# Optimization experiments

Hardware: AMD Instinct MI355X
Metric: run time of the kernel (lower is better)

## Reference

```python
import jax, jax.numpy as jnp
import numpy as np

N, D_IN, D_HID, D_OUT = 16384, 512, 2048, 512
NUM_BANDS, RANK, ALPHA = 4, 16, 32
SCALING = ALPHA / RANK  # 2.0


def setup_inputs() -> dict:
    key = jax.random.key(0)
    ks = jax.random.split(key, 10)
    x = jax.random.normal(ks[0], (N, D_IN), dtype=jnp.float32)
    bw = jax.random.uniform(ks[1], (N, NUM_BANDS), dtype=jnp.float32)
    band_weights = bw / jnp.sum(bw, axis=-1, keepdims=True)  # rows sum to 1
    s_in = 1.0 / np.sqrt(D_IN)
    s_hid = 1.0 / np.sqrt(D_HID)
    return {
        "x": x,
        "band_weights": band_weights,
        "W1": jax.random.normal(ks[2], (D_IN, D_HID), dtype=jnp.float32) * s_in,
        "b1": jax.random.normal(ks[3], (D_HID,), dtype=jnp.float32) * 0.01,
        "W2": jax.random.normal(ks[4], (D_HID, D_OUT), dtype=jnp.float32) * s_hid,
        "b2": jax.random.normal(ks[5], (D_OUT,), dtype=jnp.float32) * 0.01,
        "lora_fc1_A": jax.random.normal(ks[6], (NUM_BANDS, D_IN, RANK), dtype=jnp.float32) * s_in,
        "lora_fc1_B": jax.random.normal(ks[7], (NUM_BANDS, RANK, D_HID), dtype=jnp.float32) * 0.02,
        "lora_fc2_A": jax.random.normal(ks[8], (NUM_BANDS, D_HID, RANK), dtype=jnp.float32) * s_hid,
        "lora_fc2_B": jax.random.normal(ks[9], (NUM_BANDS, RANK, D_OUT), dtype=jnp.float32) * 0.02,
    }


def reference(x, band_weights, W1, b1, W2, b2, lora_fc1_A, lora_fc1_B, lora_fc2_A, lora_fc2_B):
    # shared fc1: [N, hidden]
    h_shared = x @ W1 + b1
    # per-band LoRA down-projection: [N, bands, rank]
    t1 = jnp.einsum('ni,bir->nbr', x, lora_fc1_A)
    # up-project and band-weighted sum fused: [N, hidden]
    delta1 = jnp.einsum('nb,nbr,brh->nh', band_weights, t1, lora_fc1_B) * SCALING
    h = jax.nn.gelu(h_shared + delta1, approximate=False)  # torch GELU is erf-based
    out_shared = h @ W2 + b2
    t2 = jnp.einsum('nh,bhr->nbr', h, lora_fc2_A)
    delta2 = jnp.einsum('nb,nbr,bro->no', band_weights, t2, lora_fc2_B) * SCALING
    return out_shared + delta2
```

## Files before the change

### kernel.cpp

```cpp
#include <hip/hip_runtime.h>
#include <hip/hip_bf16.h>

#define DEV __device__ __forceinline__
#define AS1 __attribute__((address_space(1)))
#define AS3 __attribute__((address_space(3)))

typedef __attribute__((ext_vector_type(8))) short bf16x8;
typedef __attribute__((ext_vector_type(4))) float f32x4;

static constexpr int NR   = 16384;
static constexpr int DIN  = 512;
static constexpr int DHID = 2048;
static constexpr int DOUT = 512;
static constexpr int LR   = 64;
static constexpr int K1   = DIN + LR;
static constexpr int K2   = DHID + LR;

DEV unsigned short f2bf(float f) {
  unsigned u = __float_as_uint(f);
  u += 0x7fffu + ((u >> 16) & 1u);
  return (unsigned short)(u >> 16);
}

DEV float fast_gelu(float v) {
  float x2 = v * v;
  float a  = -v * __builtin_fmaf(0.10294324f, x2, 2.30220817f);
  float t  = exp2f(a);
  return v * __builtin_amdgcn_rcpf(1.0f + t);
}

template<int N> DEV void wvm() {
  asm volatile("s_waitcnt vmcnt(%0)" :: "i"(N) : "memory");
}

DEV void tconv_dev(const float* in, unsigned short* out, int C, int LDO, int CO,
                   int bx, int by, float (*t)[33], int tid) {
  int bc = bx * 32, br = by * 32;
  int tx = tid & 31, ty = tid >> 5;
  #pragma unroll
  for (int i = 0; i < 32; i += 8)
    t[ty + i][tx] = in[(size_t)(br + ty + i) * C + bc + tx];
  __syncthreads();
  #pragma unroll
  for (int i = 0; i < 32; i += 8)
    out[(size_t)(bc + ty + i) * LDO + CO + br + tx] = f2bf(t[tx][ty + i]);
}

__global__ __launch_bounds__(256) void prep_kernel(
    const float* __restrict__ W1, const float* __restrict__ B1,
    const float* __restrict__ W2, const float* __restrict__ B2,
    unsigned short* __restrict__ W1cT, unsigned short* __restrict__ W2cT,
    const float* __restrict__ A1, const float* __restrict__ A2,
    unsigned short* __restrict__ A1T, unsigned short* __restrict__ A2T) {
  __shared__ float t[32][33];
  const int b = blockIdx.x, tid = threadIdx.x;
  if (b < 1024) {
    tconv_dev(W1, W1cT, 2048, K1, 0, b & 63, b >> 6, t, tid);
  } else if (b < 2048) {
    int bi = b - 1024;
    tconv_dev(W2, W2cT, 512, K2, 0, bi & 15, bi >> 4, t, tid);
  } else if (b < 2176) {
    int bi = b - 2048;
    tconv_dev(B1, W1cT, 2048, K1, 512, bi & 63, bi >> 6, t, tid);
  } else if (b < 2208) {
    int bi = b - 2176;
    tconv_dev(B2, W2cT, 512, K2, 2048, bi & 15, bi >> 4, t, tid);
  } else if (b < 2336) {
    int i2 = (b - 2208) * 256 + tid;
    int j = i2 / DIN, i = i2 - j * DIN;
    A1T[i2] = f2bf(A1[((size_t)(j >> 4) * DIN + i) * 16 + (j & 15)]);
  } else {
    int i2 = (b - 2336) * 256 + tid;
    int j = i2 / DHID, i = i2 - j * DHID;
    A2T[i2] = f2bf(A2[((size_t)(j >> 4) * DHID + i) * 16 + (j & 15)]);
  }
}

__global__ __launch_bounds__(256) void u1cvt_kernel(
    const float* __restrict__ x, const float* __restrict__ bw,
    const unsigned short* __restrict__ A1T, unsigned short* __restrict__ xaug) {
  __shared__ __align__(16) unsigned short lX[64 * 64];
  __shared__ __align__(16) unsigned short lW[64 * 64];
  const int tid = threadIdx.x;
  const int w = tid >> 6, lane = tid & 63;
  const int bm = blockIdx.x * 64;
  const int l15 = lane & 15;
  const int kc0 = ((lane >> 4) ^ (lane & 7)) * 8;
  const int kc1 = (((lane >> 4) + 4) ^ (lane & 7)) * 8;

  f32x4 acc[4] = {};

  for (int kt = 0; kt < 8; ++kt) {
    #pragma unroll
    for (int i = 0; i < 2; ++i) {
      int row = i * 32 + w * 8 + (lane >> 3);
      __builtin_amdgcn_global_load_lds(
          (const AS1 void*)(A1T + (size_t)row * DIN + kt * 64
                              + (((lane & 7) ^ (row & 7)) * 8)),
          (AS3 void*)(lW + (i * 32 + w * 8) * 64 + lane * 8), 16, 0, 0);
    }
    #pragma unroll
    for (int p = 0; p < 4; ++p) {
      int row = p * 16 + (tid >> 4);
      int col = (tid & 15) * 4;
      float4 v = *(const float4*)(x + (size_t)(bm + row) * DIN + kt * 64 + col);
      uint2 o;
      o.x = (unsigned)f2bf(v.x) | ((unsigned)f2bf(v.y) << 16);
      o.y = (unsigned)f2bf(v.z) | ((unsigned)f2bf(v.w) << 16);
      *(uint2*)(xaug + (size_t)(bm + row) * K1 + kt * 64 + col) = o;
      char* p3 = (char*)lX + row * 128 + (((col >> 3) ^ (row & 7)) << 4) + ((col & 7) << 1);
      *(uint2*)p3 = o;
    }
    __syncthreads();
    bf16x8 af0 = *(const bf16x8*)(lX + (w * 16 + l15) * 64 + kc0);
    bf16x8 af1 = *(const bf16x8*)(lX + (w * 16 + l15) * 64 + kc1);
    #pragma unroll
    for (int n = 0; n < 4; ++n) {
      bf16x8 b0 = *(const bf16x8*)(lW + (n * 16 + l15) * 64 + kc0);
      bf16x8 b1 = *(const bf16x8*)(lW + (n * 16 + l15) * 64 + kc1);
      acc[n] = __builtin_amdgcn_mfma_f32_16x16x32_bf16(af0, b0, acc[n], 0, 0, 0);
      acc[n] = __builtin_amdgcn_mfma_f32_16x16x32_bf16(af1, b1, acc[n], 0, 0, 0);
    }
    __syncthreads();
  }

  #pragma unroll
  for (int n = 0; n < 4; ++n) {
    int col = n * 16 + l15;
    #pragma unroll
    for (int r = 0; r < 4; ++r) {
      int row = bm + w * 16 + ((lane >> 4) << 2) + r;
      float v = acc[n][r] * 2.0f * bw[row * 4 + n];
      xaug[(size_t)row * K1 + 512 + col] = f2bf(v);
    }
  }
}

template<int BM, int BN, int WAVES, int K, int EPI, int NBY>
__global__ __launch_bounds__(WAVES * 64, 2) void gemmx_kernel(
    const unsigned short* __restrict__ A, int lda,
    const unsigned short* __restrict__ B, int ldb,
    const float* __restrict__ bias,
    void* __restrict__ outp, int ldo, int ocol) {
  constexpr int THREADS = WAVES * 64;
  constexpr int NT = K / 64;
  constexpr int AL = BM * 4 / THREADS;
  constexpr int BL = BN * 4 / THREADS;
  constexpr int HA = (BM / 2) * 64;
  constexpr int HB = (BN / 2) * 64;
  constexpr int MQ = BM / 64;
  constexpr int WC = WAVES / 2;
  static_assert(NT >= 2 && AL >= 1 && BL >= 1 && (BN / 2) / WC == 32, "geometry");
  __shared__ __align__(16) unsigned short lA[4 * HA];
  __shared__ __align__(16) unsigned short lB[4 * HB];

  const int tid  = threadIdx.x;
  const int w    = tid >> 6, lane = tid & 63;
  const int wr   = w / WC, wc = w % WC;
  const int bid  = blockIdx.x;
  const int tt   = bid >> 3;
  const int by   = tt % NBY;
  const int bx   = (tt / NBY) * 8 + (bid & 7);
  const int bm   = bx * BM, bn = by * BN;
  const int l15  = lane & 15;
  const int kc0  = ((lane >> 4) ^ (lane & 7)) * 8;
  const int kc1  = (((lane >> 4) + 4) ^ (lane & 7)) * 8;

  f32x4 acc[2][2][MQ][2] = {};
  bf16x8 af[2][MQ][2];
  bf16x8 bfv[2][2];

  auto stageA = [&](int buf, int half, int t) {
    #pragma unroll
    for (int i = 0; i < AL; ++i) {
      int row = w * (AL * 8) + i * 8 + (lane >> 3);
      __builtin_amdgcn_global_load_lds(
          (const AS1 void*)(A + (size_t)(bm + half * (BM / 2) + row) * lda
                              + (size_t)t * 64 + (((lane & 7) ^ (row & 7)) * 8)),
          (AS3 void*)(lA + (buf * 2 + half) * HA + (w * AL + i) * 512),
          16, 0, 0);
    }
  };
  auto stageB = [&](int buf, int half, int t) {
    #pragma unroll
    for (int i = 0; i < BL; ++i) {
      int row = w * (BL * 8) + i * 8 + (lane >> 3);
      __builtin_amdgcn_global_load_lds(
          (const AS1 void*)(B + (size_t)(bn + half * (BN / 2) + row) * ldb
                              + (size_t)t * 64 + (((lane & 7) ^ (row & 7)) * 8)),
          (AS3 void*)(lB + (buf * 2 + half) * HB + (w * BL + i) * 512),
          16, 0, 0);
    }
  };
  auto ldAall = [&](int buf) {
    #pragma unroll
    for (int mh = 0; mh < 2; ++mh) {
      const unsigned short* sA = lA + (buf * 2 + mh) * HA;
      #pragma unroll
      for (int m = 0; m < MQ; ++m) {
        int ro = (wr * (BM / 4) + m * 16 + l15) * 64;
        af[mh][m][0] = *(const bf16x8*)(sA + ro + kc0);
        af[mh][m][1] = *(const bf16x8*)(sA + ro + kc1);
      }
    }
  };
  auto ldB = [&](int buf, int nh) {
    const unsigned short* sB = lB + (buf * 2 + nh) * HB;
    #pragma unroll
    for (int n = 0; n < 2; ++n) {
      int ro = (wc * 32 + n * 16 + l15) * 64;
      bfv[n][0] = *(const bf16x8*)(sB + ro + kc0);
      bfv[n][1] = *(const bf16x8*)(sB + ro + kc1);
    }
  };

#define MFMA_Q(mh, nh)                                                           \
  _Pragma("unroll")                                                              \
  for (int m = 0; m < MQ; ++m)                                                   \
    _Pragma("unroll")                                                            \
    for (int n = 0; n < 2; ++n) {                                                \
      acc[mh][nh][m][n] = __builtin_amdgcn_mfma_f32_16x16x32_bf16(               \
          af[mh][m][0], bfv[n][0], acc[mh][nh][m][n], 0, 0, 0);                  \
      acc[mh][nh][m][n] = __builtin_amdgcn_mfma_f32_16x16x32_bf16(               \
          af[mh][m][1], bfv[n][1], acc[mh][nh][m][n], 0, 0, 0);                  \
    }

#define BAR() __builtin_amdgcn_s_barrier()

  stageA(0, 0, 0); stageA(0, 1, 0); stageB(0, 0, 0); stageB(0, 1, 0);
  wvm<BL>();
  BAR();

  for (int t = 0; t < NT; ++t) {
    const int buf = t & 1, nb = buf ^ 1;
    const bool more = (t + 1 < NT);
    ldAall(buf);
    ldB(buf, 0);
    if (more) { stageA(nb, 0, t + 1); stageA(nb, 1, t + 1); stageB(nb, 0, t + 1); }
    MFMA_Q(0, 0);
    MFMA_Q(1, 0);
    if (more) wvm<2 * AL + BL>(); else wvm<0>();
    BAR();
    if (more) stageB(nb, 1, t + 1);
    ldB(buf, 1);
    MFMA_Q(0, 1);
    MFMA_Q(1, 1);
    if (more) {
      wvm<BL>();
      BAR();
    }
  }
#undef MFMA_Q
#undef BAR

  float biasv[2][2];
  #pragma unroll
  for (int nh = 0; nh < 2; ++nh)
    #pragma unroll
    for (int n = 0; n < 2; ++n)
      biasv[nh][n] = bias[bn + nh * (BN / 2) + wc * 32 + n * 16 + l15];

  #pragma unroll
  for (int mh = 0; mh < 2; ++mh)
    #pragma unroll
    for (int nh = 0; nh < 2; ++nh)
      #pragma unroll
      for (int m = 0; m < MQ; ++m)
        #pragma unroll
        for (int n = 0; n < 2; ++n) {
          int col  = bn + nh * (BN / 2) + wc * 32 + n * 16 + l15;
          int rowb = bm + mh * (BM / 2) + wr * (BM / 4) + m * 16 + ((lane >> 4) << 2);
          #pragma unroll
          for (int r = 0; r < 4; ++r) {
            float v = acc[mh][nh][m][n][r];
            int row = rowb + r;
            if (EPI == 0) {
              v = fast_gelu(v + biasv[nh][n]);
              ((unsigned short*)outp)[(size_t)row * ldo + ocol + col] = f2bf(v);
            } else {
              v += biasv[nh][n];
              ((float*)outp)[(size_t)row * ldo + col] = v;
            }
          }
        }
}

template<int BM, int BN, int WM, int WN, int K>
__global__ __launch_bounds__(256) void gemmu_kernel(
    const unsigned short* __restrict__ A, int lda,
    const unsigned short* __restrict__ B, int ldb,
    const float* __restrict__ bw,
    unsigned short* __restrict__ outp, int ldo, int ocol) {
  constexpr int WRM = WM / 16, WRN = WN / 16;
  constexpr int NWN = BN / WN;
  constexpr int NT  = K / 64;
  constexpr int NBUF = 3;
  constexpr int AISS = BM * 64 * 2 / 4096;
  constexpr int BISS = BN * 64 * 2 / 4096;
  constexpr int LOADS = AISS + BISS;
  static_assert((BM / WM) * (BN / WN) == 4 && NT >= NBUF, "geometry");
  __shared__ __align__(16) unsigned short lA[NBUF * BM * 64];
  __shared__ __align__(16) unsigned short lB[NBUF * BN * 64];

  const int tid  = threadIdx.x;
  const int wid  = tid >> 6, lane = tid & 63;
  const int wr   = wid / NWN, wc = wid % NWN;
  const int bm   = blockIdx.x * BM, bn = blockIdx.y * BN;
  const int l15  = lane & 15;
  const int kc0  = ((lane >> 4) ^ (lane & 7)) * 8;
  const int kc1  = (((lane >> 4) + 4) ^ (lane & 7)) * 8;

  f32x4 acc[WRM][WRN] = {};

  auto stage = [&](int buf, int t) {
    #pragma unroll
    for (int i = 0; i < AISS; i++) {
      int row = (wid * AISS + i) * 8 + (lane >> 3);
      __builtin_amdgcn_global_load_lds(
          (const AS1 void*)(A + (size_t)(bm + row) * lda + (size_t)t * 64
                              + (((lane & 7) ^ (row & 7)) * 8)),
          (AS3 void*)(lA + buf * (BM * 64) + (wid * AISS + i) * 512), 16, 0, 0);
    }
    #pragma unroll
    for (int i = 0; i < BISS; i++) {
      int row = (wid * BISS + i) * 8 + (lane >> 3);
      __builtin_amdgcn_global_load_lds(
          (const AS1 void*)(B + (size_t)(bn + row) * ldb + (size_t)t * 64
                              + (((lane & 7) ^ (row & 7)) * 8)),
          (AS3 void*)(lB + buf * (BN * 64) + (wid * BISS + i) * 512), 16, 0, 0);
    }
  };
  auto compute = [&](int buf) {
    const unsigned short* pA = lA + buf * (BM * 64);
    const unsigned short* pB = lB + buf * (BN * 64);
    bf16x8 af[WRM][2], bfv[WRN][2];
    #pragma unroll
    for (int m = 0; m < WRM; m++) {
      int ro = (wr * WM + m * 16 + l15) * 64;
      af[m][0] = *(const bf16x8*)(pA + ro + kc0);
      af[m][1] = *(const bf16x8*)(pA + ro + kc1);
    }
    #pragma unroll
    for (int n = 0; n < WRN; n++) {
      int ro = (wc * WN + n * 16 + l15) * 64;
      bfv[n][0] = *(const bf16x8*)(pB + ro + kc0);
      bfv[n][1] = *(const bf16x8*)(pB + ro + kc1);
    }
    #pragma unroll
    for (int m = 0; m < WRM; m++)
      #pragma unroll
      for (int n = 0; n < WRN; n++) {
        acc[m][n] = __builtin_amdgcn_mfma_f32_16x16x32_bf16(af[m][0], bfv[n][0], acc[m][n], 0, 0, 0);
        acc[m][n] = __builtin_amdgcn_mfma_f32_16x16x32_bf16(af[m][1], bfv[n][1], acc[m][n], 0, 0, 0);
      }
  };

  stage(0, 0); stage(1, 1); stage(2, 2);
  wvm<2 * LOADS>();
  __builtin_amdgcn_s_barrier();

  int bt = 0;
  for (int t = 0; t < NT; ++t) {
    compute(bt);
    __builtin_amdgcn_s_barrier();
    if (t + 1 < NT) {
      if (t + NBUF < NT) stage(bt, t + NBUF);
      int newer = (t + NBUF < NT) ? (NBUF - 1) : (NT - 2 - t);
      if (newer >= 2)      wvm<2 * LOADS>();
      else if (newer == 1) wvm<LOADS>();
      else                 wvm<0>();
      __builtin_amdgcn_s_barrier();
      bt = (bt == NBUF - 1) ? 0 : bt + 1;
    }
  }

  const int r0 = bm + wr * WM;
  const int c0 = bn + wc * WN;
  #pragma unroll
  for (int m = 0; m < WRM; m++)
    #pragma unroll
    for (int n = 0; n < WRN; n++) {
      int col  = c0 + n * 16 + l15;
      int rowb = r0 + m * 16 + ((lane >> 4) << 2);
      #pragma unroll
      for (int r = 0; r < 4; r++) {
        float v = acc[m][n][r] * 2.0f * bw[(rowb + r) * 4 + (col >> 4)];
        outp[(size_t)(rowb + r) * ldo + ocol + col] = f2bf(v);
      }
    }
}

extern "C" void kernel_launch(void* const* d_in, const int* in_sizes, int n_in,
                              void* d_out, int out_size, void* d_ws, size_t ws_size,
                              hipStream_t stream) {
  const float* x  = (const float*)d_in[0];
  const float* bw = (const float*)d_in[1];
  const float* W1 = (const float*)d_in[2];
  const float* b1 = (const float*)d_in[3];
  const float* W2 = (const float*)d_in[4];
  const float* b2 = (const float*)d_in[5];
  const float* A1 = (const float*)d_in[6];
  const float* B1 = (const float*)d_in[7];
  const float* A2 = (const float*)d_in[8];
  const float* B2 = (const float*)d_in[9];
  float* out = (float*)d_out;

  char* w = (char*)d_ws;
  unsigned short* xaug = (unsigned short*)w;  w += (size_t)NR * K1 * 2;
  unsigned short* haug = (unsigned short*)w;  w += (size_t)NR * K2 * 2;
  unsigned short* W1cT = (unsigned short*)w;  w += (size_t)DHID * K1 * 2;
  unsigned short* W2cT = (unsigned short*)w;  w += (size_t)DOUT * K2 * 2;
  unsigned short* A1T  = (unsigned short*)w;  w += (size_t)64 * DIN * 2;
  unsigned short* A2T  = (unsigned short*)w;  w += (size_t)64 * DHID * 2;

  prep_kernel<<<2848, 256, 0, stream>>>(W1, B1, W2, B2, W1cT, W2cT, A1, A2, A1T, A2T);
  u1cvt_kernel<<<NR / 64, 256, 0, stream>>>(x, bw, A1T, xaug);
  gemmx_kernel<256, 256, 8, K1, 0, 8><<<dim3(512), 512, 0, stream>>>(
      xaug, K1, W1cT, K1, b1, haug, K2, 0);
  gemmu_kernel<64, 64, 32, 32, 2048><<<dim3(NR / 64, 1), 256, 0, stream>>>(
      haug, K2, A2T, DHID, bw, haug, K2, 2048);
  gemmx_kernel<128, 256, 8, K2, 1, 2><<<dim3(256), 512, 0, stream>>>(
      haug, K2, W2cT, K2, b2, out, DOUT, 0);
}
```

Measured before the change: 138.0 us.

## Fuse fc2 LoRA down-projection into the fc2 GEMM kernel

```diff
diff --git a/kernel.cpp b/kernel.cpp
--- a/kernel.cpp
+++ b/kernel.cpp
@@ -32,6 +32,7 @@
 template<int N> DEV void wvm() {
   asm volatile("s_waitcnt vmcnt(%0)" :: "i"(N) : "memory");
 }
+DEV void wlgkm0() { asm volatile("s_waitcnt lgkmcnt(0)" ::: "memory"); }
 
 DEV void tconv_dev(const float* in, unsigned short* out, int C, int LDO, int CO,
                    int bx, int by, float (*t)[33], int tid) {
@@ -136,12 +137,12 @@
   }
 }
 
-template<int BM, int BN, int WAVES, int K, int EPI, int NBY>
+template<int BM, int BN, int WAVES, int K, int NBY>
 __global__ __launch_bounds__(WAVES * 64, 2) void gemmx_kernel(
     const unsigned short* __restrict__ A, int lda,
     const unsigned short* __restrict__ B, int ldb,
     const float* __restrict__ bias,
-    void* __restrict__ outp, int ldo, int ocol) {
+    unsigned short* __restrict__ outp, int ldo) {
   constexpr int THREADS = WAVES * 64;
   constexpr int NT = K / 64;
   constexpr int AL = BM * 4 / THREADS;
@@ -272,122 +273,211 @@
           int rowb = bm + mh * (BM / 2) + wr * (BM / 4) + m * 16 + ((lane >> 4) << 2);
           #pragma unroll
           for (int r = 0; r < 4; ++r) {
-            float v = acc[mh][nh][m][n][r];
-            int row = rowb + r;
-            if (EPI == 0) {
-              v = fast_gelu(v + biasv[nh][n]);
-              ((unsigned short*)outp)[(size_t)row * ldo + ocol + col] = f2bf(v);
-            } else {
-              v += biasv[nh][n];
-              ((float*)outp)[(size_t)row * ldo + col] = v;
-            }
+            float v = fast_gelu(acc[mh][nh][m][n][r] + biasv[nh][n]);
+            outp[(size_t)(rowb + r) * ldo + col] = f2bf(v);
           }
         }
 }
 
-template<int BM, int BN, int WM, int WN, int K>
-__global__ __launch_bounds__(256) void gemmu_kernel(
+template<int NBY>
+__global__ __launch_bounds__(512, 2) void gemm2f_kernel(
     const unsigned short* __restrict__ A, int lda,
     const unsigned short* __restrict__ B, int ldb,
-    const float* __restrict__ bw,
-    unsigned short* __restrict__ outp, int ldo, int ocol) {
-  constexpr int WRM = WM / 16, WRN = WN / 16;
-  constexpr int NWN = BN / WN;
-  constexpr int NT  = K / 64;
-  constexpr int NBUF = 3;
-  constexpr int AISS = BM * 64 * 2 / 4096;
-  constexpr int BISS = BN * 64 * 2 / 4096;
-  constexpr int LOADS = AISS + BISS;
-  static_assert((BM / WM) * (BN / WN) == 4 && NT >= NBUF, "geometry");
-  __shared__ __align__(16) unsigned short lA[NBUF * BM * 64];
-  __shared__ __align__(16) unsigned short lB[NBUF * BN * 64];
+    const unsigned short* __restrict__ U,
+    const float* __restrict__ bias, const float* __restrict__ bw,
+    float* __restrict__ outp, int ldo) {
+  constexpr int BM = 128, BN = 256;
+  constexpr int NTH = DHID / 64;
+  constexpr int AL = 1, BL = 2;
+  constexpr int HA = (BM / 2) * 64;
+  constexpr int HB = (BN / 2) * 64;
+  constexpr int MQ = BM / 64;
+  constexpr int WC = 4;
+  __shared__ __align__(16) unsigned short lA[4 * HA];
+  __shared__ __align__(16) unsigned short lB[4 * HB];
+  __shared__ __align__(16) unsigned short lU[2 * 4096];
 
   const int tid  = threadIdx.x;
-  const int wid  = tid >> 6, lane = tid & 63;
-  const int wr   = wid / NWN, wc = wid % NWN;
-  const int bm   = blockIdx.x * BM, bn = blockIdx.y * BN;
+  const int w    = tid >> 6, lane = tid & 63;
+  const int wr   = w / WC, wc = w % WC;
+  const int bid  = blockIdx.x;
+  const int tt   = bid >> 3;
+  const int by   = tt % NBY;
+  const int bx   = (tt / NBY) * 8 + (bid & 7);
+  const int bm   = bx * BM, bn = by * BN;
   const int l15  = lane & 15;
   const int kc0  = ((lane >> 4) ^ (lane & 7)) * 8;
   const int kc1  = (((lane >> 4) + 4) ^ (lane & 7)) * 8;
 
-  f32x4 acc[WRM][WRN] = {};
-
-  auto stage = [&](int buf, int t) {
-    #pragma unroll
-    for (int i = 0; i < AISS; i++) {
-      int row = (wid * AISS + i) * 8 + (lane >> 3);
+  f32x4 acc[2][2][MQ][2] = {};
+  f32x4 uacc[2][MQ] = {};
+  bf16x8 af[2][MQ][2];
+  bf16x8 bfv[2][2];
+  bf16x8 bu[2];
+
+  auto stageA = [&](int buf, int half, int t) {
+    int row = w * 8 + (lane >> 3);
+    __builtin_amdgcn_global_load_lds(
+        (const AS1 void*)(A + (size_t)(bm + half * 64 + row) * lda
+                            + (size_t)t * 64 + (((lane & 7) ^ (row & 7)) * 8)),
+        (AS3 void*)(lA + (buf * 2 + half) * HA + w * 512),
+        16, 0, 0);
+  };
+  auto stageB = [&](int buf, int half, int t) {
+    #pragma unroll
+    for (int i = 0; i < BL; ++i) {
+      int row = w * 16 + i * 8 + (lane >> 3);
       __builtin_amdgcn_global_load_lds(
-          (const AS1 void*)(A + (size_t)(bm + row) * lda + (size_t)t * 64
-                              + (((lane & 7) ^ (row & 7)) * 8)),
-          (AS3 void*)(lA + buf * (BM * 64) + (wid * AISS + i) * 512), 16, 0, 0);
-    }
-    #pragma unroll
-    for (int i = 0; i < BISS; i++) {
-      int row = (wid * BISS + i) * 8 + (lane >> 3);
-      __builtin_amdgcn_global_load_lds(
-          (const AS1 void*)(B + (size_t)(bn + row) * ldb + (size_t)t * 64
-                              + (((lane & 7) ^ (row & 7)) * 8)),
-          (AS3 void*)(lB + buf * (BN * 64) + (wid * BISS + i) * 512), 16, 0, 0);
-    }
-  };
-  auto compute = [&](int buf) {
-    const unsigned short* pA = lA + buf * (BM * 64);
-    const unsigned short* pB = lB + buf * (BN * 64);
-    bf16x8 af[WRM][2], bfv[WRN][2];
-    #pragma unroll
-    for (int m = 0; m < WRM; m++) {
-      int ro = (wr * WM + m * 16 + l15) * 64;
-      af[m][0] = *(const bf16x8*)(pA + ro + kc0);
-      af[m][1] = *(const bf16x8*)(pA + ro + kc1);
-    }
-    #pragma unroll
-    for (int n = 0; n < WRN; n++) {
-      int ro = (wc * WN + n * 16 + l15) * 64;
-      bfv[n][0] = *(const bf16x8*)(pB + ro + kc0);
-      bfv[n][1] = *(const bf16x8*)(pB + ro + kc1);
-    }
-    #pragma unroll
-    for (int m = 0; m < WRM; m++)
-      #pragma unroll
-      for (int n = 0; n < WRN; n++) {
-        acc[m][n] = __builtin_amdgcn_mfma_f32_16x16x32_bf16(af[m][0], bfv[n][0], acc[m][n], 0, 0, 0);
-        acc[m][n] = __builtin_amdgcn_mfma_f32_16x16x32_bf16(af[m][1], bfv[n][1], acc[m][n], 0, 0, 0);
+          (const AS1 void*)(B + (size_t)(bn + half * 128 + row) * ldb
+                              + (size_t)t * 64 + (((lane & 7) ^ (row & 7)) * 8)),
+          (AS3 void*)(lB + (buf * 2 + half) * HB + (w * BL + i) * 512),
+          16, 0, 0);
+    }
+  };
+  auto stageU = [&](int buf, int t) {
+    int row = w * 8 + (lane >> 3);
+    __builtin_amdgcn_global_load_lds(
+        (const AS1 void*)(U + (size_t)row * DHID
+                            + (size_t)t * 64 + (((lane & 7) ^ (row & 7)) * 8)),
+        (AS3 void*)(lU + buf * 4096 + w * 512),
+        16, 0, 0);
+  };
+  auto ldAall = [&](int buf) {
+    #pragma unroll
+    for (int mh = 0; mh < 2; ++mh) {
+      const unsigned short* sA = lA + (buf * 2 + mh) * HA;
+      #pragma unroll
+      for (int m = 0; m < MQ; ++m) {
+        int ro = (wr * 32 + m * 16 + l15) * 64;
+        af[mh][m][0] = *(const bf16x8*)(sA + ro + kc0);
+        af[mh][m][1] = *(const bf16x8*)(sA + ro + kc1);
       }
-  };
-
-  stage(0, 0); stage(1, 1); stage(2, 2);
-  wvm<2 * LOADS>();
-  __builtin_amdgcn_s_barrier();
-
-  int bt = 0;
-  for (int t = 0; t < NT; ++t) {
-    compute(bt);
-    __builtin_amdgcn_s_barrier();
-    if (t + 1 < NT) {
-      if (t + NBUF < NT) stage(bt, t + NBUF);
-      int newer = (t + NBUF < NT) ? (NBUF - 1) : (NT - 2 - t);
-      if (newer >= 2)      wvm<2 * LOADS>();
-      else if (newer == 1) wvm<LOADS>();
-      else                 wvm<0>();
-      __builtin_amdgcn_s_barrier();
-      bt = (bt == NBUF - 1) ? 0 : bt + 1;
+    }
+  };
+  auto ldB = [&](int buf, int nh) {
+    const unsigned short* sB = lB + (buf * 2 + nh) * HB;
+    #pragma unroll
+    for (int n = 0; n < 2; ++n) {
+      int ro = (wc * 32 + n * 16 + l15) * 64;
+      bfv[n][0] = *(const bf16x8*)(sB + ro + kc0);
+      bfv[n][1] = *(const bf16x8*)(sB + ro + kc1);
+    }
+  };
+  auto ldU = [&](int buf) {
+    const unsigned short* sU = lU + buf * 4096;
+    int ro = (wc * 16 + l15) * 64;
+    bu[0] = *(const bf16x8*)(sU + ro + kc0);
+    bu[1] = *(const bf16x8*)(sU + ro + kc1);
+  };
+
+#define MFMA_Q(mh, nh)                                                           \
+  _Pragma("unroll")                                                              \
+  for (int m = 0; m < MQ; ++m)                                                   \
+    _Pragma("unroll")                                                            \
+    for (int n = 0; n < 2; ++n) {                                                \
+      acc[mh][nh][m][n] = __builtin_amdgcn_mfma_f32_16x16x32_bf16(               \
+          af[mh][m][0], bfv[n][0], acc[mh][nh][m][n], 0, 0, 0);                  \
+      acc[mh][nh][m][n] = __builtin_amdgcn_mfma_f32_16x16x32_bf16(               \
+          af[mh][m][1], bfv[n][1], acc[mh][nh][m][n], 0, 0, 0);                  \
+    }
+
+#define BAR() __builtin_amdgcn_s_barrier()
+
+  stageA(0, 0, 0); stageA(0, 1, 0); stageB(0, 0, 0); stageU(0, 0); stageB(0, 1, 0);
+  wvm<2>();
+  BAR();
+
+  for (int t = 0; t < NTH; ++t) {
+    const int buf = t & 1, nb = buf ^ 1;
+    const bool more = (t + 1 < NTH);
+    ldAall(buf);
+    ldB(buf, 0);
+    ldU(buf);
+    if (more) {
+      stageA(nb, 0, t + 1); stageA(nb, 1, t + 1); stageB(nb, 0, t + 1); stageU(nb, t + 1);
+    } else {
+      stageB(nb, 0, NTH); stageB(nb, 1, NTH);
+    }
+    MFMA_Q(0, 0);
+    MFMA_Q(1, 0);
+    #pragma unroll
+    for (int mh = 0; mh < 2; ++mh)
+      #pragma unroll
+      for (int m = 0; m < MQ; ++m) {
+        uacc[mh][m] = __builtin_amdgcn_mfma_f32_16x16x32_bf16(af[mh][m][0], bu[0], uacc[mh][m], 0, 0, 0);
+        uacc[mh][m] = __builtin_amdgcn_mfma_f32_16x16x32_bf16(af[mh][m][1], bu[1], uacc[mh][m], 0, 0, 0);
+      }
+    if (more) wvm<5>(); else wvm<4>();
+    BAR();
+    if (more) stageB(nb, 1, t + 1);
+    ldB(buf, 1);
+    MFMA_Q(0, 1);
+    MFMA_Q(1, 1);
+    if (more) {
+      wvm<2>();
+      BAR();
     }
   }
 
-  const int r0 = bm + wr * WM;
-  const int c0 = bn + wc * WN;
-  #pragma unroll
-  for (int m = 0; m < WRM; m++)
-    #pragma unroll
-    for (int n = 0; n < WRN; n++) {
-      int col  = c0 + n * 16 + l15;
-      int rowb = r0 + m * 16 + ((lane >> 4) << 2);
-      #pragma unroll
-      for (int r = 0; r < 4; r++) {
-        float v = acc[m][n][r] * 2.0f * bw[(rowb + r) * 4 + (col >> 4)];
-        outp[(size_t)(rowb + r) * ldo + ocol + col] = f2bf(v);
+  #pragma unroll
+  for (int mh = 0; mh < 2; ++mh)
+    #pragma unroll
+    for (int m = 0; m < MQ; ++m)
+      #pragma unroll
+      for (int r = 0; r < 4; ++r) {
+        int row = mh * 64 + wr * 32 + m * 16 + ((lane >> 4) << 2) + r;
+        float v = uacc[mh][m][r] * 2.0f * bw[(size_t)(bm + row) * 4 + wc];
+        int kcol = wc * 16 + l15;
+        *(unsigned short*)((char*)lU + row * 128
+            + ((((kcol >> 3) ^ (row & 7))) << 4) + ((kcol & 7) << 1)) = f2bf(v);
       }
-    }
+  wvm<0>();
+  wlgkm0();
+  BAR();
+
+  {
+    const int fbuf = (NTH - 1) & 1 ? 0 : 1;
+    #pragma unroll
+    for (int mh = 0; mh < 2; ++mh) {
+      const unsigned short* sA = lU + mh * 4096;
+      #pragma unroll
+      for (int m = 0; m < MQ; ++m) {
+        int ro = (wr * 32 + m * 16 + l15) * 64;
+        af[mh][m][0] = *(const bf16x8*)(sA + ro + kc0);
+        af[mh][m][1] = *(const bf16x8*)(sA + ro + kc1);
+      }
+    }
+    ldB(fbuf, 0);
+    MFMA_Q(0, 0);
+    MFMA_Q(1, 0);
+    ldB(fbuf, 1);
+    MFMA_Q(0, 1);
+    MFMA_Q(1, 1);
+  }
+#undef MFMA_Q
+#undef BAR
+
+  float biasv[2][2];
+  #pragma unroll
+  for (int nh = 0; nh < 2; ++nh)
+    #pragma unroll
+    for (int n = 0; n < 2; ++n)
+      biasv[nh][n] = bias[bn + nh * 128 + wc * 32 + n * 16 + l15];
+
+  #pragma unroll
+  for (int mh = 0; mh < 2; ++mh)
+    #pragma unroll
+    for (int nh = 0; nh < 2; ++nh)
+      #pragma unroll
+      for (int m = 0; m < MQ; ++m)
+        #pragma unroll
+        for (int n = 0; n < 2; ++n) {
+          int col  = bn + nh * 128 + wc * 32 + n * 16 + l15;
+          int rowb = bm + mh * 64 + wr * 32 + m * 16 + ((lane >> 4) << 2);
+          #pragma unroll
+          for (int r = 0; r < 4; ++r)
+            outp[(size_t)(rowb + r) * ldo + col] = acc[mh][nh][m][n][r] + biasv[nh][n];
+        }
 }
 
 extern "C" void kernel_launch(void* const* d_in, const int* in_sizes, int n_in,
@@ -407,7 +497,7 @@
 
   char* w = (char*)d_ws;
   unsigned short* xaug = (unsigned short*)w;  w += (size_t)NR * K1 * 2;
-  unsigned short* haug = (unsigned short*)w;  w += (size_t)NR * K2 * 2;
+  unsigned short* haug = (unsigned short*)w;  w += (size_t)NR * DHID * 2;
   unsigned short* W1cT = (unsigned short*)w;  w += (size_t)DHID * K1 * 2;
   unsigned short* W2cT = (unsigned short*)w;  w += (size_t)DOUT * K2 * 2;
   unsigned short* A1T  = (unsigned short*)w;  w += (size_t)64 * DIN * 2;
@@ -415,10 +505,8 @@
 
   prep_kernel<<<2848, 256, 0, stream>>>(W1, B1, W2, B2, W1cT, W2cT, A1, A2, A1T, A2T);
   u1cvt_kernel<<<NR / 64, 256, 0, stream>>>(x, bw, A1T, xaug);
-  gemmx_kernel<256, 256, 8, K1, 0, 8><<<dim3(512), 512, 0, stream>>>(
-      xaug, K1, W1cT, K1, b1, haug, K2, 0);
-  gemmu_kernel<64, 64, 32, 32, 2048><<<dim3(NR / 64, 1), 256, 0, stream>>>(
-      haug, K2, A2T, DHID, bw, haug, K2, 2048);
-  gemmx_kernel<128, 256, 8, K2, 1, 2><<<dim3(256), 512, 0, stream>>>(
-      haug, K2, W2cT, K2, b2, out, DOUT, 0);
-}
+  gemmx_kernel<256, 256, 8, K1, 8><<<dim3(512), 512, 0, stream>>>(
+      xaug, K1, W1cT, K1, b1, haug, DHID);
+  gemm2f_kernel<2><<<dim3(256), 512, 0, stream>>>(
+      haug, DHID, W2cT, K2, A2T, b2, bw, out, DOUT);
+}
```

After: 119.9 us. -13.1%, faster.
